# Kernel tuning notes

Measured on AMD Instinct MI355X. Metric: run time of the kernel, lower is better.

The kernel has to match this reference:

```python
import jax, jax.numpy as jnp
import numpy as np

HEADS = 8
DIM_HEAD = 64
SCALE = DIM_HEAD ** -0.5


def setup_inputs() -> dict:
    key = jax.random.key(0)
    k1, k2, k3 = jax.random.split(key, 3)
    b, n, dim = 2, 4096, 512
    inner = HEADS * DIM_HEAD  # 512
    x = jax.random.normal(k1, (b, n, dim), dtype=jnp.float32)
    # torch Linear weight is [out, in]; store transposed [in, out] for x @ W
    w_qkv = jax.random.normal(k2, (dim, inner), dtype=jnp.float32) * (dim ** -0.5)
    w_out = jax.random.normal(k3, (inner, dim), dtype=jnp.float32) * (inner ** -0.5)
    b_out = jnp.zeros((dim,), dtype=jnp.float32)
    return {"x": x, "w_qkv": w_qkv, "w_out": w_out, "b_out": b_out}


def reference(x, w_qkv, w_out, b_out):
    b, n, _ = x.shape
    # shared projection: w acts as q = k = v
    w = (x @ w_qkv).reshape(b, n, HEADS, DIM_HEAD).transpose(0, 2, 1, 3)  # b h n d
    dots = jnp.einsum('bhid,bhjd->bhij', w, w) * SCALE                    # b h n n
    attn = jax.nn.softmax(dots, axis=-1)
    out = jnp.einsum('bhij,bhjd->bhid', attn, w)                          # b h n d
    out = out.transpose(0, 2, 1, 3).reshape(b, n, HEADS * DIM_HEAD)       # b n (h d)
    return out @ w_out + b_out
```

## Files before the change

kernel.cpp:

```cpp
#include <hip/hip_runtime.h>

typedef __attribute__((ext_vector_type(8))) short short8;
typedef __attribute__((ext_vector_type(8))) unsigned short u16x8;
typedef __attribute__((ext_vector_type(4))) float f32x4;
typedef __attribute__((ext_vector_type(16))) float f32x16;
typedef __attribute__((ext_vector_type(4))) unsigned int u32x4;

#define MFMA16 __builtin_amdgcn_mfma_f32_16x16x32_bf16
#define MFMA32 __builtin_amdgcn_mfma_f32_32x32x16_bf16

__device__ __forceinline__ unsigned short f2bf(float f) {
  unsigned int u = __builtin_bit_cast(unsigned int, f);
  u = (u + 0x7FFFu + ((u >> 16) & 1u)) >> 16;
  return (unsigned short)u;
}

__device__ __forceinline__ unsigned int cvt_pk_bf16(float lo, float hi) {
  unsigned int r;
  asm("v_cvt_pk_bf16_f32 %0, %1, %2" : "=v"(r) : "v"(lo), "v"(hi));
  return r;
}

__device__ __forceinline__ void pl32_swap(unsigned int& a, unsigned int& b) {
  asm("v_permlane32_swap_b32 %0, %1" : "+v"(a), "+v"(b));
}

__device__ __forceinline__ float exp2_raw(float x) {
  float r;
  asm("v_exp_f32 %0, %1" : "=v"(r) : "v"(x));
  return r;
}

#define GLOAD_LDS16(g, l)                                                   \
  __builtin_amdgcn_global_load_lds(                                         \
      (const __attribute__((address_space(1))) unsigned int*)(g),           \
      (__attribute__((address_space(3))) unsigned int*)(l), 16, 0, 0)


__global__ __launch_bounds__(256) void san_qkv(const float* __restrict__ x,
                                               const float* __restrict__ wqkv,
                                               unsigned short* __restrict__ wf,
                                               unsigned short* __restrict__ vtf) {
  __shared__ unsigned short Alds[128 * 40];
  __shared__ unsigned short Blds[64 * 40];
  const int t = threadIdx.x;
  const int m0 = (blockIdx.x >> 3) * 128;
  const int n0 = (blockIdx.x & 7) * 64;
  const int lane = t & 63, wv = t >> 6;
  const int wr = wv >> 1, wc = wv & 1;
  const int lr = lane & 15, lg = lane >> 4;

  f32x4 acc[4][2];
  #pragma unroll
  for (int m = 0; m < 4; ++m)
    #pragma unroll
    for (int n = 0; n < 2; ++n) acc[m][n] = (f32x4){0.f, 0.f, 0.f, 0.f};

  for (int k0 = 0; k0 < 512; k0 += 32) {
    __syncthreads();
    {
      const int row = t >> 1, c0 = (t & 1) * 16;
      const float* src = x + (m0 + row) * 512 + k0 + c0;
      unsigned short tmp[16];
      #pragma unroll
      for (int i = 0; i < 4; ++i) {
        f32x4 v = *(const f32x4*)(src + i * 4);
        #pragma unroll
        for (int e = 0; e < 4; ++e) tmp[i * 4 + e] = f2bf(v[e]);
      }
      *(u16x8*)&Alds[row * 40 + c0]     = *(u16x8*)&tmp[0];
      *(u16x8*)&Alds[row * 40 + c0 + 8] = *(u16x8*)&tmp[8];
    }
    {
      const int k = t & 31, nb = (t >> 5) * 8;
      const float* src = wqkv + (k0 + k) * 512 + n0 + nb;
      #pragma unroll
      for (int i = 0; i < 8; i += 4) {
        f32x4 v = *(const f32x4*)(src + i);
        #pragma unroll
        for (int e = 0; e < 4; ++e) Blds[(nb + i + e) * 40 + k] = f2bf(v[e]);
      }
    }
    __syncthreads();
    short8 af[4], bfr[2];
    #pragma unroll
    for (int m = 0; m < 4; ++m)
      af[m] = *(const short8*)&Alds[(wr * 64 + m * 16 + lr) * 40 + lg * 8];
    #pragma unroll
    for (int n = 0; n < 2; ++n)
      bfr[n] = *(const short8*)&Blds[(wc * 32 + n * 16 + lr) * 40 + lg * 8];
    #pragma unroll
    for (int m = 0; m < 4; ++m)
      #pragma unroll
      for (int n = 0; n < 2; ++n)
        acc[m][n] = MFMA16(af[m], bfr[n], acc[m][n], 0, 0, 0);
  }
  #pragma unroll
  for (int m = 0; m < 4; ++m)
    #pragma unroll
    for (int n = 0; n < 2; ++n) {
      int gcol = n0 + wc * 32 + n * 16 + lr;
      int h = gcol >> 6, d = gcol & 63;
      int grow0 = m0 + wr * 64 + m * 16 + lg * 4;
      int b = grow0 >> 12, nn0 = grow0 & 4095;
      size_t hb = (size_t)((b << 3) + h);
      size_t tbase = (hb << 18) + ((size_t)(nn0 >> 6) << 12);
      int sd = d >> 4, hid = (d >> 3) & 1, e = d & 7;
      #pragma unroll
      for (int r = 0; r < 4; ++r) {
        int nn = nn0 + r;
        int jh = (nn >> 5) & 1;
        int l  = (nn & 31) | (hid << 5);
        wf[tbase + (size_t)((((jh << 2) + sd) << 9) + (l << 3) + e)] =
            f2bf(acc[m][n][r]);
      }
      unsigned int p0 = cvt_pk_bf16(acc[m][n][0], acc[m][n][1]);
      unsigned int p1 = cvt_pk_bf16(acc[m][n][2], acc[m][n][3]);
      int dh = d >> 5, sj = (nn0 >> 4) & 3;
      int lv = (d & 31) | (((nn0 >> 3) & 1) << 5);
      unsigned short* vp =
          vtf + tbase + (size_t)((((dh << 2) + sj) << 9) + (lv << 3) + (nn0 & 7));
      *(unsigned int*)(vp)     = p0;
      *(unsigned int*)(vp + 2) = p1;
    }
}

__global__ __launch_bounds__(512, 4) void san_attn(
    const unsigned short* __restrict__ wf, const unsigned short* __restrict__ vtf,
    unsigned short* __restrict__ o) {
  __shared__ char smem[65536];
  const int t = threadIdx.x;
  const int lane = t & 63, wp = t >> 6;
  const int lo5 = lane & 31, hi = lane >> 5;
  const int qg = wp & 3, kvhalf = wp >> 2;
  const int bid = blockIdx.x;
  const int bh = ((bid & 7) << 1) + ((bid >> 3) & 1);
  const int qblk = bid >> 4;
  const unsigned short* whf = wf + ((size_t)bh << 18);
  const unsigned short* wthf = vtf + ((size_t)bh << 18);

  const int qrow = qblk * 128 + qg * 32 + lo5;
  const int jtq = qrow >> 6, jhq = (qrow >> 5) & 1;
  const unsigned short* qb = whf + ((size_t)jtq << 12) + ((jhq << 2) << 9) +
                             (((qrow & 31) | (hi << 5)) << 3);
  short8 qf0 = *(const short8*)(qb + 0 * 512);
  short8 qf1 = *(const short8*)(qb + 1 * 512);
  short8 qf2 = *(const short8*)(qb + 2 * 512);
  short8 qf3 = *(const short8*)(qb + 3 * 512);

  f32x16 oacc0, oacc1, fz;
  #pragma unroll
  for (int r = 0; r < 16; ++r) { oacc0[r] = 0.f; oacc1[r] = 0.f; fz[r] = 0.f; }
  float l_run = 0.f;
  const float cE = 0.125f * 1.4426950408889634f;
  const float nmnc = -28.8539008178f;

  auto stage = [&](int buf, int jt) {
    #pragma unroll
    for (int h = 0; h < 2; ++h) {
      int gt = h * 32 + jt;
      const char* ksrc = (const char*)whf + ((size_t)gt << 13) + t * 16;
      GLOAD_LDS16(ksrc, smem + (buf * 2 + h) * 8192 + t * 16);
      const char* vsrc = (const char*)wthf + ((size_t)gt << 13) + t * 16;
      GLOAD_LDS16(vsrc, smem + 32768 + (buf * 2 + h) * 8192 + t * 16);
    }
  };

  auto computeTile = [&](const char* kb, const char* vb) {
    f32x16 st0, st1;
    __builtin_amdgcn_s_setprio(1);
    {
      short8 k0v = *(const short8*)(kb + 0 * 1024 + lane * 16);
      short8 k1v = *(const short8*)(kb + 1 * 1024 + lane * 16);
      short8 k2v = *(const short8*)(kb + 2 * 1024 + lane * 16);
      short8 k3v = *(const short8*)(kb + 3 * 1024 + lane * 16);
      st0 = MFMA32(k0v, qf0, fz, 0, 0, 0);
      st0 = MFMA32(k1v, qf1, st0, 0, 0, 0);
      st0 = MFMA32(k2v, qf2, st0, 0, 0, 0);
      st0 = MFMA32(k3v, qf3, st0, 0, 0, 0);
    }
    {
      short8 k0v = *(const short8*)(kb + 4096 + 0 * 1024 + lane * 16);
      short8 k1v = *(const short8*)(kb + 4096 + 1 * 1024 + lane * 16);
      short8 k2v = *(const short8*)(kb + 4096 + 2 * 1024 + lane * 16);
      short8 k3v = *(const short8*)(kb + 4096 + 3 * 1024 + lane * 16);
      st1 = MFMA32(k0v, qf0, fz, 0, 0, 0);
      st1 = MFMA32(k1v, qf1, st1, 0, 0, 0);
      st1 = MFMA32(k2v, qf2, st1, 0, 0, 0);
      st1 = MFMA32(k3v, qf3, st1, 0, 0, 0);
    }
    __builtin_amdgcn_s_setprio(0);

    float ps0 = 0.f, ps1 = 0.f, ps2 = 0.f, ps3 = 0.f;
    #pragma unroll
    for (int r = 0; r < 16; ++r) {
      float p = exp2_raw(__builtin_fmaf(st0[r], cE, nmnc));
      st0[r] = p;
      if ((r & 3) == 0) ps0 += p; else if ((r & 3) == 1) ps1 += p;
      else if ((r & 3) == 2) ps2 += p; else ps3 += p;
    }
    #pragma unroll
    for (int r = 0; r < 16; ++r) {
      float p = exp2_raw(__builtin_fmaf(st1[r], cE, nmnc));
      st1[r] = p;
      if ((r & 3) == 0) ps0 += p; else if ((r & 3) == 1) ps1 += p;
      else if ((r & 3) == 2) ps2 += p; else ps3 += p;
    }
    l_run += (ps0 + ps1) + (ps2 + ps3);

    unsigned int c0 = cvt_pk_bf16(st0[0], st0[1]);
    unsigned int c1 = cvt_pk_bf16(st0[2], st0[3]);
    unsigned int c2 = cvt_pk_bf16(st0[4], st0[5]);
    unsigned int c3 = cvt_pk_bf16(st0[6], st0[7]);
    unsigned int c4 = cvt_pk_bf16(st0[8], st0[9]);
    unsigned int c5 = cvt_pk_bf16(st0[10], st0[11]);
    unsigned int c6 = cvt_pk_bf16(st0[12], st0[13]);
    unsigned int c7 = cvt_pk_bf16(st0[14], st0[15]);
    pl32_swap(c0, c2); pl32_swap(c1, c3);
    pl32_swap(c4, c6); pl32_swap(c5, c7);
    u32x4 u0 = {c0, c1, c2, c3}, u1 = {c4, c5, c6, c7};
    short8 pf0 = __builtin_bit_cast(short8, u0);
    short8 pf1 = __builtin_bit_cast(short8, u1);
    c0 = cvt_pk_bf16(st1[0], st1[1]);
    c1 = cvt_pk_bf16(st1[2], st1[3]);
    c2 = cvt_pk_bf16(st1[4], st1[5]);
    c3 = cvt_pk_bf16(st1[6], st1[7]);
    c4 = cvt_pk_bf16(st1[8], st1[9]);
    c5 = cvt_pk_bf16(st1[10], st1[11]);
    c6 = cvt_pk_bf16(st1[12], st1[13]);
    c7 = cvt_pk_bf16(st1[14], st1[15]);
    pl32_swap(c0, c2); pl32_swap(c1, c3);
    pl32_swap(c4, c6); pl32_swap(c5, c7);
    u32x4 u2 = {c0, c1, c2, c3}, u3 = {c4, c5, c6, c7};
    short8 pf2 = __builtin_bit_cast(short8, u2);
    short8 pf3 = __builtin_bit_cast(short8, u3);

    __builtin_amdgcn_s_setprio(1);
    #pragma unroll
    for (int s = 0; s < 4; ++s) {
      short8 vfr = *(const short8*)(vb + s * 1024 + lane * 16);
      oacc0 = MFMA32(vfr, (s == 0 ? pf0 : s == 1 ? pf1 : s == 2 ? pf2 : pf3), oacc0, 0, 0, 0);
    }
    #pragma unroll
    for (int s = 0; s < 4; ++s) {
      short8 vfr = *(const short8*)(vb + 4096 + s * 1024 + lane * 16);
      oacc1 = MFMA32(vfr, (s == 0 ? pf0 : s == 1 ? pf1 : s == 2 ? pf2 : pf3), oacc1, 0, 0, 0);
    }
    __builtin_amdgcn_s_setprio(0);
  };

  auto kbuf = [&](int buf) { return (const char*)(smem + (buf * 2 + kvhalf) * 8192); };
  auto vbuf = [&](int buf) { return (const char*)(smem + 32768 + (buf * 2 + kvhalf) * 8192); };

  stage(0, 0);
  __syncthreads();
  for (int jt = 0; jt < 32; jt += 2) {
    stage(1, jt + 1);
    computeTile(kbuf(0), vbuf(0));
    __syncthreads();
    if (jt + 2 < 32) stage(0, jt + 2);
    computeTile(kbuf(1), vbuf(1));
    __syncthreads();
  }

  float l_tot = l_run + __shfl_xor(l_run, 32);

  float* scratch = (float*)smem;
  float* obase = scratch + qg * 2112;
  if (kvhalf == 1) {
    #pragma unroll
    for (int c = 0; c < 4; ++c) {
      f32x4 v = {oacc0[4 * c], oacc0[4 * c + 1], oacc0[4 * c + 2], oacc0[4 * c + 3]};
      *(f32x4*)(obase + c * 256 + lane * 4) = v;
    }
    #pragma unroll
    for (int c = 0; c < 4; ++c) {
      f32x4 v = {oacc1[4 * c], oacc1[4 * c + 1], oacc1[4 * c + 2], oacc1[4 * c + 3]};
      *(f32x4*)(obase + 1024 + c * 256 + lane * 4) = v;
    }
    obase[2048 + lane] = l_tot;
  }
  __syncthreads();
  if (kvhalf == 0) {
    float l_b = obase[2048 + lane];
    float linv = 1.f / (l_tot + l_b);
    float ob0[16], ob1[16];
    #pragma unroll
    for (int c = 0; c < 4; ++c) {
      f32x4 v = *(const f32x4*)(obase + c * 256 + lane * 4);
      #pragma unroll
      for (int e = 0; e < 4; ++e) ob0[4 * c + e] = v[e];
    }
    #pragma unroll
    for (int c = 0; c < 4; ++c) {
      f32x4 v = *(const f32x4*)(obase + 1024 + c * 256 + lane * 4);
      #pragma unroll
      for (int e = 0; e < 4; ++e) ob1[4 * c + e] = v[e];
    }
    unsigned short* oh = o + (size_t)bh * (4096 * 64);
    #pragma unroll
    for (int i = 0; i < 8; ++i) {
      float a0 = (oacc0[2 * i] + ob0[2 * i]) * linv;
      float a1 = (oacc0[2 * i + 1] + ob0[2 * i + 1]) * linv;
      float b0 = (oacc1[2 * i] + ob1[2 * i]) * linv;
      float b1 = (oacc1[2 * i + 1] + ob1[2 * i + 1]) * linv;
      unsigned int pk0 = cvt_pk_bf16(a0, a1);
      unsigned int pk1 = cvt_pk_bf16(b0, b1);
      int dl = ((2 * i) & 3) + 8 * ((2 * i) >> 2) + 4 * hi;
      *(unsigned int*)(oh + qrow * 64 + dl) = pk0;
      *(unsigned int*)(oh + qrow * 64 + 32 + dl) = pk1;
    }
  }
}

__global__ __launch_bounds__(256) void san_out(const unsigned short* __restrict__ o,
                                               const float* __restrict__ wo,
                                               const float* __restrict__ bias,
                                               float* __restrict__ out) {
  __shared__ unsigned short Alds[128 * 40];
  __shared__ unsigned short Blds[64 * 40];
  const int t = threadIdx.x;
  const int m0 = (blockIdx.x >> 3) * 128;
  const int n0 = (blockIdx.x & 7) * 64;
  const int lane = t & 63, wv = t >> 6;
  const int wr = wv >> 1, wc = wv & 1;
  const int lr = lane & 15, lg = lane >> 4;

  f32x4 acc[4][2];
  #pragma unroll
  for (int m = 0; m < 4; ++m)
    #pragma unroll
    for (int n = 0; n < 2; ++n) acc[m][n] = (f32x4){0.f, 0.f, 0.f, 0.f};

  for (int k0 = 0; k0 < 512; k0 += 32) {
    __syncthreads();
    {
      const int row = t >> 1, seg = t & 1;
      int grow = m0 + row;
      int b = grow >> 12, nn = grow & 4095;
      int h = k0 >> 6;
      int dbase = (k0 & 63) + seg * 16;
      const unsigned short* src =
          o + ((size_t)((b << 3) + h) * 4096 + nn) * 64 + dbase;
      *(u16x8*)&Alds[row * 40 + seg * 16]     = *(const u16x8*)src;
      *(u16x8*)&Alds[row * 40 + seg * 16 + 8] = *(const u16x8*)(src + 8);
    }
    {
      const int k = t & 31, nb = (t >> 5) * 8;
      const float* src = wo + (k0 + k) * 512 + n0 + nb;
      #pragma unroll
      for (int i = 0; i < 8; i += 4) {
        f32x4 v = *(const f32x4*)(src + i);
        #pragma unroll
        for (int e = 0; e < 4; ++e) Blds[(nb + i + e) * 40 + k] = f2bf(v[e]);
      }
    }
    __syncthreads();
    short8 af[4], bfr[2];
    #pragma unroll
    for (int m = 0; m < 4; ++m)
      af[m] = *(const short8*)&Alds[(wr * 64 + m * 16 + lr) * 40 + lg * 8];
    #pragma unroll
    for (int n = 0; n < 2; ++n)
      bfr[n] = *(const short8*)&Blds[(wc * 32 + n * 16 + lr) * 40 + lg * 8];
    #pragma unroll
    for (int m = 0; m < 4; ++m)
      #pragma unroll
      for (int n = 0; n < 2; ++n)
        acc[m][n] = MFMA16(af[m], bfr[n], acc[m][n], 0, 0, 0);
  }
  #pragma unroll
  for (int m = 0; m < 4; ++m)
    #pragma unroll
    for (int n = 0; n < 2; ++n)
      #pragma unroll
      for (int r = 0; r < 4; ++r) {
        int grow = m0 + wr * 64 + m * 16 + lg * 4 + r;
        int gcol = n0 + wc * 32 + n * 16 + lr;
        out[(size_t)grow * 512 + gcol] = acc[m][n][r] + bias[gcol];
      }
}

extern "C" void kernel_launch(void* const* d_in, const int* in_sizes, int n_in,
                              void* d_out, int out_size, void* d_ws, size_t ws_size,
                              hipStream_t stream) {
  const float* x    = (const float*)d_in[0];
  const float* wqkv = (const float*)d_in[1];
  const float* wo   = (const float*)d_in[2];
  const float* bias = (const float*)d_in[3];
  float* out = (float*)d_out;

  unsigned short* wff = (unsigned short*)d_ws;
  unsigned short* wso = wff + (size_t)2 * 8 * 4096 * 64;
  unsigned short* vtf = wso + (size_t)2 * 8 * 4096 * 64;

  san_qkv<<<dim3(512), dim3(256), 0, stream>>>(x, wqkv, wff, vtf);
  san_attn<<<dim3(512), dim3(512), 0, stream>>>(wff, vtf, wso);
  san_out<<<dim3(512), dim3(256), 0, stream>>>(wso, wo, bias, out);
}
```

Measured before the change: 127.6 us.

## Pre-convert GEMM operands to bf16 MFMA-fragment layout and double-buffer LDS

Adds a prep kernel that converts x and w_qkv to bf16 once, laid out in the per-lane MFMA fragment order, using the output buffer as scratch. The QKV and output-projection GEMMs then stage tiles with direct global-to-LDS loads and double buffering, and the attention kernel writes its output directly in the fragment layout that the output GEMM reads. This removes the redundant per-block fp32-to-bf16 conversion and the padded LDS transposes, and lets loads overlap with MFMA work. The cost is an extra kernel launch plus an extra pass over x through memory.

```diff
diff --git a/kernel.cpp b/kernel.cpp
--- a/kernel.cpp
+++ b/kernel.cpp
@@ -37,15 +37,43 @@
       (__attribute__((address_space(3))) unsigned int*)(l), 16, 0, 0)
 
 
-__global__ __launch_bounds__(256) void san_qkv(const float* __restrict__ x,
-                                               const float* __restrict__ wqkv,
+__global__ __launch_bounds__(256) void san_prep(const float* __restrict__ x,
+                                                const float* __restrict__ wqkv,
+                                                unsigned short* __restrict__ xf,
+                                                unsigned short* __restrict__ qkf) {
+  const int bid = blockIdx.x, t = threadIdx.x;
+  if (bid < 2048) {
+    int cid = bid * 256 + t;
+    int l = cid & 63, msub = (cid >> 6) & 7, kt = (cid >> 9) & 15, mt = cid >> 13;
+    int row = mt * 128 + msub * 16 + (l & 15);
+    int col = kt * 32 + (l >> 4) * 8;
+    const float* src = x + (size_t)row * 512 + col;
+    f32x4 v0 = *(const f32x4*)(src);
+    f32x4 v1 = *(const f32x4*)(src + 4);
+    unsigned short tmp[8];
+    #pragma unroll
+    for (int e = 0; e < 4; ++e) { tmp[e] = f2bf(v0[e]); tmp[4 + e] = f2bf(v1[e]); }
+    *(u16x8*)(xf + (size_t)cid * 8) = *(u16x8*)tmp;
+  } else {
+    int c = (bid - 2048) * 256 + t;
+    int l = c & 63, nsub = (c >> 6) & 3, kt = (c >> 8) & 15, nt = c >> 12;
+    int n = nt * 64 + nsub * 16 + (l & 15);
+    int k0 = kt * 32 + (l >> 4) * 8;
+    unsigned short tmp[8];
+    #pragma unroll
+    for (int e = 0; e < 8; ++e) tmp[e] = f2bf(wqkv[(size_t)(k0 + e) * 512 + n]);
+    *(u16x8*)(qkf + (size_t)c * 8) = *(u16x8*)tmp;
+  }
+}
+
+__global__ __launch_bounds__(256) void san_qkv(const unsigned short* __restrict__ xf,
+                                               const unsigned short* __restrict__ qkf,
                                                unsigned short* __restrict__ wf,
                                                unsigned short* __restrict__ vtf) {
-  __shared__ unsigned short Alds[128 * 40];
-  __shared__ unsigned short Blds[64 * 40];
+  __shared__ char smem[24576];
   const int t = threadIdx.x;
-  const int m0 = (blockIdx.x >> 3) * 128;
-  const int n0 = (blockIdx.x & 7) * 64;
+  const int mt = blockIdx.x >> 3, nt = blockIdx.x & 7;
+  const int m0 = mt * 128, n0 = nt * 64;
   const int lane = t & 63, wv = t >> 6;
   const int wr = wv >> 1, wc = wv & 1;
   const int lr = lane & 15, lg = lane >> 4;
@@ -56,45 +84,38 @@
     #pragma unroll
     for (int n = 0; n < 2; ++n) acc[m][n] = (f32x4){0.f, 0.f, 0.f, 0.f};
 
-  for (int k0 = 0; k0 < 512; k0 += 32) {
-    __syncthreads();
-    {
-      const int row = t >> 1, c0 = (t & 1) * 16;
-      const float* src = x + (m0 + row) * 512 + k0 + c0;
-      unsigned short tmp[16];
-      #pragma unroll
-      for (int i = 0; i < 4; ++i) {
-        f32x4 v = *(const f32x4*)(src + i * 4);
-        #pragma unroll
-        for (int e = 0; e < 4; ++e) tmp[i * 4 + e] = f2bf(v[e]);
-      }
-      *(u16x8*)&Alds[row * 40 + c0]     = *(u16x8*)&tmp[0];
-      *(u16x8*)&Alds[row * 40 + c0 + 8] = *(u16x8*)&tmp[8];
-    }
-    {
-      const int k = t & 31, nb = (t >> 5) * 8;
-      const float* src = wqkv + (k0 + k) * 512 + n0 + nb;
-      #pragma unroll
-      for (int i = 0; i < 8; i += 4) {
-        f32x4 v = *(const f32x4*)(src + i);
-        #pragma unroll
-        for (int e = 0; e < 4; ++e) Blds[(nb + i + e) * 40 + k] = f2bf(v[e]);
-      }
-    }
-    __syncthreads();
+  auto stage = [&](int buf, int kt) {
+    const char* asrc = (const char*)xf + (((size_t)mt * 16 + kt) << 13);
+    GLOAD_LDS16(asrc + t * 16, smem + buf * 8192 + t * 16);
+    GLOAD_LDS16(asrc + 4096 + t * 16, smem + buf * 8192 + 4096 + t * 16);
+    const char* bsrc = (const char*)qkf + (((size_t)nt * 16 + kt) << 12);
+    GLOAD_LDS16(bsrc + t * 16, smem + 16384 + buf * 4096 + t * 16);
+  };
+  auto compute = [&](int buf) {
+    const char* ab = smem + buf * 8192;
+    const char* bb = smem + 16384 + buf * 4096;
     short8 af[4], bfr[2];
     #pragma unroll
     for (int m = 0; m < 4; ++m)
-      af[m] = *(const short8*)&Alds[(wr * 64 + m * 16 + lr) * 40 + lg * 8];
+      af[m] = *(const short8*)(ab + (wr * 4 + m) * 1024 + lane * 16);
     #pragma unroll
     for (int n = 0; n < 2; ++n)
-      bfr[n] = *(const short8*)&Blds[(wc * 32 + n * 16 + lr) * 40 + lg * 8];
+      bfr[n] = *(const short8*)(bb + (wc * 2 + n) * 1024 + lane * 16);
     #pragma unroll
     for (int m = 0; m < 4; ++m)
       #pragma unroll
       for (int n = 0; n < 2; ++n)
         acc[m][n] = MFMA16(af[m], bfr[n], acc[m][n], 0, 0, 0);
-  }
+  };
+
+  stage(0, 0);
+  __syncthreads();
+  for (int kt = 0; kt < 16; ++kt) {
+    if (kt + 1 < 16) stage((kt + 1) & 1, kt + 1);
+    compute(kt & 1);
+    __syncthreads();
+  }
+
   #pragma unroll
   for (int m = 0; m < 4; ++m)
     #pragma unroll
@@ -127,7 +148,7 @@
 
 __global__ __launch_bounds__(512, 4) void san_attn(
     const unsigned short* __restrict__ wf, const unsigned short* __restrict__ vtf,
-    unsigned short* __restrict__ o) {
+    unsigned short* __restrict__ of) {
   __shared__ char smem[65536];
   const int t = threadIdx.x;
   const int lane = t & 63, wp = t >> 6;
@@ -297,7 +318,10 @@
       #pragma unroll
       for (int e = 0; e < 4; ++e) ob1[4 * c + e] = v[e];
     }
-    unsigned short* oh = o + (size_t)bh * (4096 * 64);
+    const int token = ((bh >> 3) << 12) + qrow;
+    const int h = bh & 7;
+    const int mt = token >> 7, msub = (token >> 4) & 7;
+    char* ofb = (char*)of;
     #pragma unroll
     for (int i = 0; i < 8; ++i) {
       float a0 = (oacc0[2 * i] + ob0[2 * i]) * linv;
@@ -307,21 +331,23 @@
       unsigned int pk0 = cvt_pk_bf16(a0, a1);
       unsigned int pk1 = cvt_pk_bf16(b0, b1);
       int dl = ((2 * i) & 3) + 8 * ((2 * i) >> 2) + 4 * hi;
-      *(unsigned int*)(oh + qrow * 64 + dl) = pk0;
-      *(unsigned int*)(oh + qrow * 64 + 32 + dl) = pk1;
-    }
-  }
-}
-
-__global__ __launch_bounds__(256) void san_out(const unsigned short* __restrict__ o,
+      size_t addr = (((size_t)mt * 16 + h * 2) << 13) + msub * 1024 +
+                    (((token & 15) | ((dl >> 3) << 4)) << 4) + (dl & 7) * 2;
+      *(unsigned int*)(ofb + addr) = pk0;
+      *(unsigned int*)(ofb + addr + 8192) = pk1;
+    }
+  }
+}
+
+__global__ __launch_bounds__(256) void san_out(const unsigned short* __restrict__ of,
                                                const float* __restrict__ wo,
                                                const float* __restrict__ bias,
                                                float* __restrict__ out) {
-  __shared__ unsigned short Alds[128 * 40];
-  __shared__ unsigned short Blds[64 * 40];
+  __shared__ char Asm[16384];
+  __shared__ unsigned short Blds[2][64 * 40];
   const int t = threadIdx.x;
-  const int m0 = (blockIdx.x >> 3) * 128;
-  const int n0 = (blockIdx.x & 7) * 64;
+  const int mt = blockIdx.x >> 3;
+  const int m0 = mt * 128, n0 = (blockIdx.x & 7) * 64;
   const int lane = t & 63, wv = t >> 6;
   const int wr = wv >> 1, wc = wv & 1;
   const int lr = lane & 15, lg = lane >> 4;
@@ -332,43 +358,45 @@
     #pragma unroll
     for (int n = 0; n < 2; ++n) acc[m][n] = (f32x4){0.f, 0.f, 0.f, 0.f};
 
-  for (int k0 = 0; k0 < 512; k0 += 32) {
-    __syncthreads();
-    {
-      const int row = t >> 1, seg = t & 1;
-      int grow = m0 + row;
-      int b = grow >> 12, nn = grow & 4095;
-      int h = k0 >> 6;
-      int dbase = (k0 & 63) + seg * 16;
-      const unsigned short* src =
-          o + ((size_t)((b << 3) + h) * 4096 + nn) * 64 + dbase;
-      *(u16x8*)&Alds[row * 40 + seg * 16]     = *(const u16x8*)src;
-      *(u16x8*)&Alds[row * 40 + seg * 16 + 8] = *(const u16x8*)(src + 8);
-    }
-    {
-      const int k = t & 31, nb = (t >> 5) * 8;
-      const float* src = wo + (k0 + k) * 512 + n0 + nb;
-      #pragma unroll
-      for (int i = 0; i < 8; i += 4) {
-        f32x4 v = *(const f32x4*)(src + i);
-        #pragma unroll
-        for (int e = 0; e < 4; ++e) Blds[(nb + i + e) * 40 + k] = f2bf(v[e]);
-      }
-    }
-    __syncthreads();
+  auto stageA = [&](int buf, int kt) {
+    const char* asrc = (const char*)of + (((size_t)mt * 16 + kt) << 13);
+    GLOAD_LDS16(asrc + t * 16, Asm + buf * 8192 + t * 16);
+    GLOAD_LDS16(asrc + 4096 + t * 16, Asm + buf * 8192 + 4096 + t * 16);
+  };
+  auto convB = [&](int buf, int kt) {
+    const int k = t & 31, nb = (t >> 5) * 8;
+    const float* src = wo + (size_t)(kt * 32 + k) * 512 + n0 + nb;
+    #pragma unroll
+    for (int i = 0; i < 8; i += 4) {
+      f32x4 v = *(const f32x4*)(src + i);
+      #pragma unroll
+      for (int e = 0; e < 4; ++e) Blds[buf][(nb + i + e) * 40 + k] = f2bf(v[e]);
+    }
+  };
+  auto compute = [&](int buf) {
+    const char* ab = Asm + buf * 8192;
     short8 af[4], bfr[2];
     #pragma unroll
     for (int m = 0; m < 4; ++m)
-      af[m] = *(const short8*)&Alds[(wr * 64 + m * 16 + lr) * 40 + lg * 8];
+      af[m] = *(const short8*)(ab + (wr * 4 + m) * 1024 + lane * 16);
     #pragma unroll
     for (int n = 0; n < 2; ++n)
-      bfr[n] = *(const short8*)&Blds[(wc * 32 + n * 16 + lr) * 40 + lg * 8];
+      bfr[n] = *(const short8*)&Blds[buf][(wc * 32 + n * 16 + lr) * 40 + lg * 8];
     #pragma unroll
     for (int m = 0; m < 4; ++m)
       #pragma unroll
       for (int n = 0; n < 2; ++n)
         acc[m][n] = MFMA16(af[m], bfr[n], acc[m][n], 0, 0, 0);
-  }
+  };
+
+  stageA(0, 0); convB(0, 0);
+  __syncthreads();
+  for (int kt = 0; kt < 16; ++kt) {
+    if (kt + 1 < 16) { stageA((kt + 1) & 1, kt + 1); convB((kt + 1) & 1, kt + 1); }
+    compute(kt & 1);
+    __syncthreads();
+  }
+
   #pragma unroll
   for (int m = 0; m < 4; ++m)
     #pragma unroll
@@ -391,10 +419,13 @@
   float* out = (float*)d_out;
 
   unsigned short* wff = (unsigned short*)d_ws;
-  unsigned short* wso = wff + (size_t)2 * 8 * 4096 * 64;
-  unsigned short* vtf = wso + (size_t)2 * 8 * 4096 * 64;
-
-  san_qkv<<<dim3(512), dim3(256), 0, stream>>>(x, wqkv, wff, vtf);
-  san_attn<<<dim3(512), dim3(512), 0, stream>>>(wff, vtf, wso);
-  san_out<<<dim3(512), dim3(256), 0, stream>>>(wso, wo, bias, out);
-}
+  unsigned short* off = wff + (size_t)2 * 8 * 4096 * 64;
+  unsigned short* vtf = off + (size_t)2 * 8 * 4096 * 64;
+  unsigned short* xf  = (unsigned short*)d_out;
+  unsigned short* qkf = xf + (size_t)4 * 1024 * 1024;
+
+  san_prep<<<dim3(2176), dim3(256), 0, stream>>>(x, wqkv, xf, qkf);
+  san_qkv<<<dim3(512), dim3(256), 0, stream>>>(xf, qkf, wff, vtf);
+  san_attn<<<dim3(512), dim3(512), 0, stream>>>(wff, vtf, off);
+  san_out<<<dim3(512), dim3(256), 0, stream>>>(off, wo, bias, out);
+}
```

New measurement: 121.4 us (median of 2 runs). 4.8% less time.
